# Kernel tuning notes

Hardware: AMD Instinct MI355X
Metric: run time of the kernel (lower is better)

## Reference

```python
import jax, jax.numpy as jnp
import numpy as np

N_NODES = 100000
N_EDGES = 3200000
NFEAT = 512
NCLASS = 40
DIMS = [NFEAT, 256, 128, 64, NCLASS]


def _glorot(key, fan_in, fan_out):
    lim = 1.0 / np.sqrt(fan_out)
    return jax.random.uniform(key, (fan_in, fan_out), jnp.float32, -lim, lim)


def setup_inputs() -> dict:
    key = jax.random.key(0)
    ks = jax.random.split(key, 16)
    inp = {
        'x': jax.random.normal(ks[0], (N_NODES, NFEAT), jnp.float32),
        'edge_src': jax.random.randint(ks[1], (N_EDGES,), 0, N_NODES, jnp.int32),
        'edge_dst': jax.random.randint(ks[2], (N_EDGES,), 0, N_NODES, jnp.int32),
        'edge_weight': jax.random.uniform(ks[3], (N_EDGES,), jnp.float32),
    }
    for i in range(4):
        inp[f'W{i+1}'] = _glorot(ks[4 + 2 * i], DIMS[i], DIMS[i + 1])
        lim = 1.0 / np.sqrt(DIMS[i + 1])
        inp[f'b{i+1}'] = jax.random.uniform(ks[5 + 2 * i], (DIMS[i + 1],), jnp.float32, -lim, lim)
    return inp


def _gc_layer(h, W, b, src, dst, ew):
    # support = h @ W ; out = spmm(adj, support) + b
    support = h @ W                                   # [N, d_out]
    msgs = support[src] * ew[:, None]                 # gather + scale per edge
    agg = jax.ops.segment_sum(msgs, dst, num_segments=N_NODES)
    return agg + b


def reference(x, edge_src, edge_dst, edge_weight, W1, b1, W2, b2, W3, b3, W4, b4):
    h = x
    for W, b in ((W1, b1), (W2, b2), (W3, b3), (W4, b4)):
        h = jax.nn.relu(_gc_layer(h, W, b, edge_src, edge_dst, edge_weight))
    return jax.nn.log_softmax(h, axis=1)
```

## Files before the change

kernel.cpp:

```cpp
#include <hip/hip_runtime.h>
#include <hip/hip_bf16.h>
#include <math.h>
#include <stdint.h>


#define WAVE 64
#define NBK 512
#define CHA 8192
typedef __attribute__((ext_vector_type(8))) short short8;
typedef __attribute__((ext_vector_type(8))) unsigned short ushort8;
typedef __attribute__((ext_vector_type(4))) unsigned int uintx4;
typedef __attribute__((ext_vector_type(4))) float floatx4;
typedef __attribute__((ext_vector_type(2))) float floatx2;

__device__ __forceinline__ void async_copy16(const void* g, void* l) {
    __builtin_amdgcn_global_load_lds(
        (const __attribute__((address_space(1))) void*)g,
        (__attribute__((address_space(3))) void*)l, 16, 0, 0);
}

__global__ __launch_bounds__(256) void prep_weights_kernel(
        const float* __restrict__ W1, const float* __restrict__ W2,
        const float* __restrict__ W3, const float* __restrict__ W4,
        const float* __restrict__ b4,
        __hip_bfloat16* __restrict__ Wt1, __hip_bfloat16* __restrict__ Wt2,
        __hip_bfloat16* __restrict__ Wt3, __hip_bfloat16* __restrict__ Wt4,
        float* __restrict__ b4p) {
    int idx = blockIdx.x * 256 + threadIdx.x;
    if (idx < 131072) {
        int n = idx >> 9, k = idx & 511;
        Wt1[idx] = __float2bfloat16(W1[(size_t)k * 256 + n]);
    } else if (idx < 131072 + 32768) {
        int l = idx - 131072;
        int n = l >> 8, k = l & 255;
        Wt2[l] = __float2bfloat16(W2[(size_t)k * 128 + n]);
    } else if (idx < 131072 + 32768 + 8192) {
        int l = idx - 131072 - 32768;
        int n = l >> 7, k = l & 127;
        Wt3[l] = __float2bfloat16(W3[(size_t)k * 64 + n]);
    } else if (idx < 131072 + 32768 + 8192 + 4096) {
        int l = idx - 131072 - 32768 - 8192;
        int n = l >> 6, k = l & 63;
        float v = (n < 40) ? W4[(size_t)k * 40 + n] : 0.f;
        Wt4[l] = __float2bfloat16(v);
    } else if (idx < 131072 + 32768 + 8192 + 4096 + 64) {
        int l = idx - 131072 - 32768 - 8192 - 4096;
        b4p[l] = (l < 40) ? b4[l] : 0.f;
    }
}


__global__ __launch_bounds__(256) void bucket_hist(const int* __restrict__ dst,
                                                   int nE, int* __restrict__ bhist) {
    __shared__ int h[NBK];
    const int t = threadIdx.x;
    const long e0 = (long)blockIdx.x * CHA;
    const int cnt = (int)((nE - e0 < CHA) ? (nE - e0) : CHA);
    for (int i = t; i < NBK; i += 256) h[i] = 0;
    __syncthreads();
    for (int i = t; i < cnt; i += 256)
        atomicAdd(&h[dst[e0 + i] >> 8], 1);
    __syncthreads();
    for (int i = t; i < NBK; i += 256)
        if (h[i]) atomicAdd(&bhist[i], h[i]);
}

__global__ __launch_bounds__(512) void bucket_scan(const int* __restrict__ bhist,
                                                   int* __restrict__ bbase,
                                                   int* __restrict__ gcur) {
    __shared__ int sm[NBK];
    const int t = threadIdx.x;
    int x = bhist[t];
    sm[t] = x;
    __syncthreads();
    for (int off = 1; off < NBK; off <<= 1) {
        int add = (t >= off) ? sm[t - off] : 0;
        __syncthreads();
        if (t >= off) sm[t] += add;
        __syncthreads();
    }
    int excl = sm[t] - x;
    bbase[t] = excl;
    gcur[t] = excl;
    if (t == NBK - 1) bbase[NBK] = sm[t];
}

__global__ __launch_bounds__(256) void scatter_phaseA(const int* __restrict__ src,
                                                      const int* __restrict__ dst,
                                                      const float* __restrict__ ew,
                                                      int nE,
                                                      int* __restrict__ gcur,
                                                      uint2* __restrict__ E2) {
    __shared__ int hist[NBK];
    __shared__ int cur[NBK];
    const int t = threadIdx.x;
    const long e0 = (long)blockIdx.x * CHA;
    const int cnt = (int)((nE - e0 < CHA) ? (nE - e0) : CHA);

    for (int i = t; i < NBK; i += 256) hist[i] = 0;
    __syncthreads();
    for (int i = t; i < cnt; i += 256)
        atomicAdd(&hist[dst[e0 + i] >> 8], 1);
    __syncthreads();
    for (int i = t; i < NBK; i += 256) {
        int h = hist[i];
        cur[i] = h ? atomicAdd(&gcur[i], h) : 0;
    }
    __syncthreads();
    for (int i = t; i < cnt; i += 256) {
        int d = dst[e0 + i];
        unsigned int w15 = (unsigned int)(ew[e0 + i] * 32767.f + 0.5f);
        if (w15 > 32767u) w15 = 32767u;
        int pos = atomicAdd(&cur[d >> 8], 1);
        E2[pos] = make_uint2(((unsigned int)src[e0 + i] << 15) | w15,
                             (unsigned int)d);
    }
}

__global__ __launch_bounds__(256) void scatter_phaseB2(const uint2* __restrict__ E2,
                                                       const int* __restrict__ bbase,
                                                       int n_nodes, int nE,
                                                       int* __restrict__ row_ptr,
                                                       unsigned int* __restrict__ edge_pk) {
    __shared__ int cnt[256];
    __shared__ int pfx[256];
    __shared__ int cur[256];
    const int b = blockIdx.x;
    const int t = threadIdx.x;
    const int s = bbase[b];
    const int e = bbase[b + 1];

    cnt[t] = 0;
    __syncthreads();
    for (int i = s + t; i < e; i += 256)
        atomicAdd(&cnt[E2[i].y & 255], 1);
    __syncthreads();
    pfx[t] = cnt[t];
    __syncthreads();
    for (int off = 1; off < 256; off <<= 1) {
        int add = (t >= off) ? pfx[t - off] : 0;
        __syncthreads();
        if (t >= off) pfx[t] += add;
        __syncthreads();
    }
    const int excl = pfx[t] - cnt[t];
    const int node = b * 256 + t;
    if (node < n_nodes) row_ptr[node] = s + excl;
    if (b == 0 && t == 0) row_ptr[n_nodes] = nE;
    cur[t] = s + excl;
    __syncthreads();
    for (int i = s + t; i < e; i += 256) {
        uint2 ed = E2[i];
        int p = atomicAdd(&cur[ed.y & 255], 1);
        edge_pk[p] = ed.x;
    }
}


template <int AFP32, int OUTM>
__global__ __launch_bounds__(256) void gemm128(const void* __restrict__ Av,
                                               const __hip_bfloat16* __restrict__ Wt,
                                               void* __restrict__ C,
                                               int M, int K, int Npitch) {
    __shared__ __align__(16) __hip_bfloat16 sA[128 * 64];
    __shared__ __align__(16) __hip_bfloat16 sB[128 * 64];
    const int t = threadIdx.x;
    const int lane = t & 63;
    const int w = t >> 6;
    const int wy = w >> 1, wx = w & 1;
    const int quad = lane >> 4;
    const int l16 = lane & 15;

    const int nwg = (int)(gridDim.x * gridDim.y);
    const int flat = (int)(blockIdx.y * gridDim.x + blockIdx.x);
    const int q = nwg >> 3, r = nwg & 7;
    const int xcd = flat & 7, pos = flat >> 3;
    const int logical = (xcd < r ? xcd * (q + 1) : r * (q + 1) + (xcd - r) * q) + pos;
    const int row0 = (logical / (int)gridDim.x) * 128;
    const int col0 = (logical % (int)gridDim.x) * 128;

    floatx4 acc[4][4];
#pragma unroll
    for (int mt = 0; mt < 4; mt++)
#pragma unroll
        for (int nt = 0; nt < 4; nt++) acc[mt][nt] = 0;

    const int arow = t >> 3;
    const int koff = (t & 7) * 8;

    float4 fa[4][2];
    auto loadA = [&](int k0) {
#pragma unroll
        for (int rr = 0; rr < 4; rr++) {
            int gm = row0 + rr * 32 + arow;
            int gmc = (gm < M) ? gm : 0;
            const float* ap = (const float*)Av + (size_t)gmc * K + k0 + koff;
            fa[rr][0] = *(const float4*)ap;
            fa[rr][1] = *(const float4*)(ap + 4);
        }
    };
    if (AFP32) loadA(0);

    for (int k0 = 0; k0 < K; k0 += 64) {
#pragma unroll
        for (int rr = 0; rr < 4; rr++) {
            int n = rr * 32 + arow;
            async_copy16(Wt + (size_t)(col0 + n) * K + k0 + koff,
                         (char*)sB + rr * 4096 + t * 16);
        }
        if (AFP32) {
#pragma unroll
            for (int rr = 0; rr < 4; rr++) {
                ushort8 pk;
#pragma unroll
                for (int i = 0; i < 4; i++) {
                    __hip_bfloat16 b0 = __float2bfloat16(((const float*)&fa[rr][0])[i]);
                    __hip_bfloat16 b1 = __float2bfloat16(((const float*)&fa[rr][1])[i]);
                    pk[i] = *(unsigned short*)&b0;
                    pk[4 + i] = *(unsigned short*)&b1;
                }
                *(ushort8*)((char*)sA + rr * 4096 + t * 16) = pk;
            }
        } else {
#pragma unroll
            for (int rr = 0; rr < 4; rr++) {
                int gm = row0 + rr * 32 + arow;
                int gmc = (gm < M) ? gm : 0;
                async_copy16((const __hip_bfloat16*)Av + (size_t)gmc * K + k0 + koff,
                             (char*)sA + rr * 4096 + t * 16);
            }
        }
        __syncthreads();

        if (AFP32 && k0 + 64 < K) loadA(k0 + 64);

        short8 af[4][2], bfr[4][2];
#pragma unroll
        for (int mt = 0; mt < 4; mt++)
#pragma unroll
            for (int kk = 0; kk < 2; kk++)
                af[mt][kk] = *(const short8*)((const char*)sA +
                             (wy * 64 + mt * 16 + l16) * 128 + kk * 64 + quad * 16);
#pragma unroll
        for (int nt = 0; nt < 4; nt++)
#pragma unroll
            for (int kk = 0; kk < 2; kk++)
                bfr[nt][kk] = *(const short8*)((const char*)sB +
                              (wx * 64 + nt * 16 + l16) * 128 + kk * 64 + quad * 16);
#pragma unroll
        for (int kk = 0; kk < 2; kk++)
#pragma unroll
            for (int mt = 0; mt < 4; mt++)
#pragma unroll
                for (int nt = 0; nt < 4; nt++)
                    acc[mt][nt] = __builtin_amdgcn_mfma_f32_16x16x32_bf16(
                        af[mt][kk], bfr[nt][kk], acc[mt][nt], 0, 0, 0);
        __syncthreads();
    }

#pragma unroll
    for (int mt = 0; mt < 4; mt++) {
#pragma unroll
        for (int nt = 0; nt < 4; nt++) {
            int gn = col0 + wx * 64 + nt * 16 + l16;
            int gmb = row0 + wy * 64 + mt * 16 + quad * 4;
#pragma unroll
            for (int rr = 0; rr < 4; rr++) {
                int gm = gmb + rr;
                if (gm < M) {
                    if (OUTM == 0) {
                        ((__hip_bfloat16*)C)[(size_t)gm * Npitch + gn] =
                            __float2bfloat16(acc[mt][nt][rr]);
                    } else {
                        float v = acc[mt][nt][rr];
                        int p = __builtin_amdgcn_cvt_pk_fp8_f32(v, v, 0, false);
                        ((unsigned char*)C)[(size_t)gm * Npitch + gn] =
                            (unsigned char)(p & 0xff);
                    }
                }
            }
        }
    }
}


template <int OUTM>
__global__ __launch_bounds__(256) void gemm_bf16(const __hip_bfloat16* __restrict__ A,
                                                 const __hip_bfloat16* __restrict__ Wt,
                                                 void* __restrict__ C,
                                                 int M, int K, int Npitch) {
    __shared__ __align__(16) __hip_bfloat16 sA[128 * 64];
    __shared__ __align__(16) __hip_bfloat16 sB[64 * 64];
    const int t = threadIdx.x;
    const int lane = t & 63;
    const int w = t >> 6;
    const int wy = w >> 1, wx = w & 1;
    const int quad = lane >> 4;
    const int l16 = lane & 15;
    const int row0 = blockIdx.y * 128;
    const int col0 = blockIdx.x * 64;

    floatx4 acc[4][2];
#pragma unroll
    for (int mt = 0; mt < 4; mt++)
#pragma unroll
        for (int nt = 0; nt < 2; nt++) acc[mt][nt] = 0;

    const int arow = t >> 3;
    const int koff = (t & 7) * 8;

    for (int k0 = 0; k0 < K; k0 += 64) {
#pragma unroll
        for (int r = 0; r < 4; r++) {
            int gm = row0 + r * 32 + arow;
            int gmc = (gm < M) ? gm : 0;
            async_copy16(A + (size_t)gmc * K + k0 + koff,
                         (char*)sA + r * 4096 + t * 16);
        }
#pragma unroll
        for (int r = 0; r < 2; r++) {
            int n = r * 32 + arow;
            async_copy16(Wt + (size_t)(col0 + n) * K + k0 + koff,
                         (char*)sB + r * 4096 + t * 16);
        }
        __syncthreads();

        short8 af[4][2], bfr[2][2];
#pragma unroll
        for (int mt = 0; mt < 4; mt++)
#pragma unroll
            for (int kk = 0; kk < 2; kk++)
                af[mt][kk] = *(const short8*)((const char*)sA +
                             (wy * 64 + mt * 16 + l16) * 128 + kk * 64 + quad * 16);
#pragma unroll
        for (int nt = 0; nt < 2; nt++)
#pragma unroll
            for (int kk = 0; kk < 2; kk++)
                bfr[nt][kk] = *(const short8*)((const char*)sB +
                              (wx * 32 + nt * 16 + l16) * 128 + kk * 64 + quad * 16);
#pragma unroll
        for (int kk = 0; kk < 2; kk++)
#pragma unroll
            for (int mt = 0; mt < 4; mt++)
#pragma unroll
                for (int nt = 0; nt < 2; nt++)
                    acc[mt][nt] = __builtin_amdgcn_mfma_f32_16x16x32_bf16(
                        af[mt][kk], bfr[nt][kk], acc[mt][nt], 0, 0, 0);
        __syncthreads();
    }

#pragma unroll
    for (int mt = 0; mt < 4; mt++) {
#pragma unroll
        for (int nt = 0; nt < 2; nt++) {
            int gn = col0 + wx * 32 + nt * 16 + l16;
            int gmb = row0 + wy * 64 + mt * 16 + quad * 4;
#pragma unroll
            for (int r = 0; r < 4; r++) {
                int gm = gmb + r;
                if (gm < M) {
                    if (OUTM == 0) {
                        ((__hip_bfloat16*)C)[(size_t)gm * Npitch + gn] =
                            __float2bfloat16(acc[mt][nt][r]);
                    } else {
                        float v = acc[mt][nt][r];
                        int p = __builtin_amdgcn_cvt_pk_fp8_f32(v, v, 0, false);
                        ((unsigned char*)C)[(size_t)gm * Npitch + gn] =
                            (unsigned char)(p & 0xff);
                    }
                }
            }
        }
    }
}


template <int D, int U, bool FINAL>
__global__ __launch_bounds__(256) void spmm_fp8(const int* __restrict__ row_ptr,
                                                const unsigned int* __restrict__ edge_pk,
                                                const unsigned char* __restrict__ sup8,
                                                const float* __restrict__ bias,
                                                void* __restrict__ out,
                                                int n_nodes) {
    constexpr int G = D / 16;
    constexpr int NG = 64 / G;
    constexpr int CH = NG * U;
    int node = blockIdx.x * (256 / WAVE) + (threadIdx.x >> 6);
    if (node >= n_nodes) return;
    node = __builtin_amdgcn_readfirstlane(node);
    const int lane = threadIdx.x & 63;
    const int g = lane / G;
    const int t = lane & (G - 1);
    int e = row_ptr[node];
    const int end = row_ptr[node + 1];
    const unsigned char* sup = sup8 + t * 16;

    float acc[16];
#pragma unroll
    for (int i = 0; i < 16; i++) acc[i] = 0.f;

    while (e < end) {
        const int base = e + g * U;
        unsigned int pk[U];
#pragma unroll
        for (int u = 0; u < U; u++) {
            int idx = base + u;
            if (idx > end - 1) idx = end - 1;
            pk[u] = edge_pk[idx];
        }
        uintx4 v[U];
#pragma unroll
        for (int u = 0; u < U; u++)
            v[u] = *(const uintx4*)(sup + (size_t)(pk[u] >> 15) * D);
#pragma unroll
        for (int u = 0; u < U; u++) {
            float wq = (float)(pk[u] & 0x7fffu) * (1.f / 32767.f);
            float wt = (base + u < end) ? wq : 0.f;
#pragma unroll
            for (int d = 0; d < 4; d++) {
                floatx2 lo = __builtin_amdgcn_cvt_pk_f32_fp8(v[u][d], false);
                floatx2 hi = __builtin_amdgcn_cvt_pk_f32_fp8(v[u][d], true);
                acc[d * 4 + 0] += lo[0] * wt;
                acc[d * 4 + 1] += lo[1] * wt;
                acc[d * 4 + 2] += hi[0] * wt;
                acc[d * 4 + 3] += hi[1] * wt;
            }
        }
        e += CH;
    }

#pragma unroll
    for (int off = G; off < 64; off <<= 1)
#pragma unroll
        for (int i = 0; i < 16; i++) acc[i] += __shfl_xor(acc[i], off);

    if (!FINAL) {
        if (lane < G) {
            ushort8 o0, o1;
#pragma unroll
            for (int i = 0; i < 8; i++) {
                float r0 = acc[i] + bias[t * 16 + i];
                float r1 = acc[8 + i] + bias[t * 16 + 8 + i];
                r0 = r0 > 0.f ? r0 : 0.f;
                r1 = r1 > 0.f ? r1 : 0.f;
                __hip_bfloat16 b0 = __float2bfloat16(r0);
                __hip_bfloat16 b1 = __float2bfloat16(r1);
                o0[i] = *(unsigned short*)&b0;
                o1[i] = *(unsigned short*)&b1;
            }
            union { ushort8 s; uintx4 u; } c0, c1; c0.s = o0; c1.s = o1;
            unsigned short* op = (unsigned short*)out + (size_t)node * D + t * 16;
            __builtin_nontemporal_store(c0.u, (uintx4*)op);
            __builtin_nontemporal_store(c1.u, (uintx4*)(op + 8));
        }
    } else {
        float r[16];
#pragma unroll
        for (int i = 0; i < 16; i++) {
            float x = acc[i] + bias[t * 16 + i];
            r[i] = x > 0.f ? x : 0.f;
        }
        float m = -INFINITY;
#pragma unroll
        for (int i = 0; i < 16; i++)
            if (t * 16 + i < 40) m = fmaxf(m, r[i]);
#pragma unroll
        for (int off = 1; off < G; off <<= 1) m = fmaxf(m, __shfl_xor(m, off));
        float s = 0.f;
#pragma unroll
        for (int i = 0; i < 16; i++)
            if (t * 16 + i < 40) s += __expf(r[i] - m);
#pragma unroll
        for (int off = 1; off < G; off <<= 1) s += __shfl_xor(s, off);
        const float lse = __logf(s);
        if (lane < G) {
            float* op = (float*)out + (size_t)node * 40;
#pragma unroll
            for (int i = 0; i < 16; i++) {
                int c = t * 16 + i;
                if (c < 40) op[c] = r[i] - m - lse;
            }
        }
    }
}


extern "C" void kernel_launch(void* const* d_in, const int* in_sizes, int n_in,
                              void* d_out, int out_size, void* d_ws, size_t ws_size,
                              hipStream_t stream) {
    const float* x    = (const float*)d_in[0];
    const int*   esrc = (const int*)d_in[1];
    const int*   edst = (const int*)d_in[2];
    const float* ew   = (const float*)d_in[3];
    const float* Wm[4] = {(const float*)d_in[4], (const float*)d_in[6],
                          (const float*)d_in[8], (const float*)d_in[10]};
    const float* bm[4] = {(const float*)d_in[5], (const float*)d_in[7],
                          (const float*)d_in[9], (const float*)d_in[11]};
    const int NFEAT = 512;
    const int n_nodes = in_sizes[0] / NFEAT;
    const int n_edges = in_sizes[1];
    float* out = (float*)d_out;

    char* wsp = (char*)d_ws;
    size_t off = 0;
    auto alloc = [&](size_t bytes) -> void* {
        void* p = wsp + off;
        off += (bytes + 255) & ~(size_t)255;
        return p;
    };
    __hip_bfloat16* Sb = (__hip_bfloat16*)alloc((size_t)n_nodes * 256 * sizeof(__hip_bfloat16));
    __hip_bfloat16* Hb = (__hip_bfloat16*)alloc((size_t)n_nodes * 256 * sizeof(__hip_bfloat16));
    __hip_bfloat16* Wt1 = (__hip_bfloat16*)alloc(256 * 512 * sizeof(__hip_bfloat16));
    __hip_bfloat16* Wt2 = (__hip_bfloat16*)alloc(128 * 256 * sizeof(__hip_bfloat16));
    __hip_bfloat16* Wt3 = (__hip_bfloat16*)alloc(64 * 128 * sizeof(__hip_bfloat16));
    __hip_bfloat16* Wt4 = (__hip_bfloat16*)alloc(64 * 64 * sizeof(__hip_bfloat16));
    float* b4p     = (float*)alloc(64 * sizeof(float));
    int*   row_ptr = (int*)alloc(((size_t)n_nodes + 1) * sizeof(int));
    int*   bhist   = (int*)alloc(NBK * sizeof(int));
    int*   bbase   = (int*)alloc((NBK + 1) * sizeof(int));
    int*   gcur    = (int*)alloc(NBK * sizeof(int));
    unsigned int* edge_pk = (unsigned int*)alloc((size_t)n_edges * sizeof(unsigned int));
    uint2* E2 = (uint2*)Hb;
    unsigned char* Sb8 = (unsigned char*)Sb;
    (void)ws_size;

    prep_weights_kernel<<<(131072 + 32768 + 8192 + 4096 + 64 + 255) / 256, 256, 0, stream>>>(
        Wm[0], Wm[1], Wm[2], Wm[3], bm[3], Wt1, Wt2, Wt3, Wt4, b4p);

    hipMemsetAsync(bhist, 0, NBK * sizeof(int), stream);
    int hblocks = (n_edges + CHA - 1) / CHA;
    bucket_hist<<<hblocks, 256, 0, stream>>>(edst, n_edges, bhist);
    bucket_scan<<<1, NBK, 0, stream>>>(bhist, bbase, gcur);
    scatter_phaseA<<<hblocks, 256, 0, stream>>>(esrc, edst, ew, n_edges, gcur, E2);
    scatter_phaseB2<<<NBK, 256, 0, stream>>>(E2, bbase, n_nodes, n_edges,
                                             row_ptr, edge_pk);

    int spmm_blocks = (n_nodes + 3) / 4;
    dim3 gg1(256 / 128, (n_nodes + 127) / 128);
    dim3 gg2(128 / 128, (n_nodes + 127) / 128);
    dim3 g3(64 / 64, (n_nodes + 127) / 128);

    gemm128<1, 1><<<gg1, 256, 0, stream>>>(x, Wt1, Sb8, n_nodes, 512, 256);
    spmm_fp8<256, 4, false><<<spmm_blocks, 256, 0, stream>>>(
        row_ptr, edge_pk, Sb8, bm[0], Hb, n_nodes);
    gemm128<0, 1><<<gg2, 256, 0, stream>>>(Hb, Wt2, Sb8, n_nodes, 256, 128);
    spmm_fp8<128, 2, false><<<spmm_blocks, 256, 0, stream>>>(
        row_ptr, edge_pk, Sb8, bm[1], Hb, n_nodes);
    gemm_bf16<1><<<g3, 256, 0, stream>>>(Hb, Wt3, Sb8, n_nodes, 128, 64);
    spmm_fp8<64, 1, false><<<spmm_blocks, 256, 0, stream>>>(
        row_ptr, edge_pk, Sb8, bm[2], Hb, n_nodes);
    gemm_bf16<1><<<g3, 256, 0, stream>>>(Hb, Wt4, Sb8, n_nodes, 64, 64);
    spmm_fp8<64, 1, true><<<spmm_blocks, 256, 0, stream>>>(
        row_ptr, edge_pk, Sb8, b4p, out, n_nodes);
}
```

Measured before the change: 817.7 us.

## Fuse edge scatter with first GEMM and histogram with weight prep

```diff
diff --git a/kernel.cpp b/kernel.cpp
--- a/kernel.cpp
+++ b/kernel.cpp
@@ -19,14 +19,29 @@
         (__attribute__((address_space(3))) void*)l, 16, 0, 0);
 }
 
-__global__ __launch_bounds__(256) void prep_weights_kernel(
+__global__ __launch_bounds__(256) void prep_hist_kernel(
+        const int* __restrict__ dst, int nE, int* __restrict__ bhist, int nH,
         const float* __restrict__ W1, const float* __restrict__ W2,
         const float* __restrict__ W3, const float* __restrict__ W4,
         const float* __restrict__ b4,
         __hip_bfloat16* __restrict__ Wt1, __hip_bfloat16* __restrict__ Wt2,
         __hip_bfloat16* __restrict__ Wt3, __hip_bfloat16* __restrict__ Wt4,
         float* __restrict__ b4p) {
-    int idx = blockIdx.x * 256 + threadIdx.x;
+    const int t = threadIdx.x;
+    if ((int)blockIdx.x < nH) {
+        __shared__ int h[NBK];
+        const long e0 = (long)blockIdx.x * CHA;
+        const int cnt = (int)((nE - e0 < CHA) ? (nE - e0) : CHA);
+        for (int i = t; i < NBK; i += 256) h[i] = 0;
+        __syncthreads();
+        for (int i = t; i < cnt; i += 256)
+            atomicAdd(&h[dst[e0 + i] >> 8], 1);
+        __syncthreads();
+        for (int i = t; i < NBK; i += 256)
+            if (h[i]) atomicAdd(&bhist[i], h[i]);
+        return;
+    }
+    int idx = ((int)blockIdx.x - nH) * 256 + t;
     if (idx < 131072) {
         int n = idx >> 9, k = idx & 511;
         Wt1[idx] = __float2bfloat16(W1[(size_t)k * 256 + n]);
@@ -49,22 +64,6 @@
     }
 }
 
-
-__global__ __launch_bounds__(256) void bucket_hist(const int* __restrict__ dst,
-                                                   int nE, int* __restrict__ bhist) {
-    __shared__ int h[NBK];
-    const int t = threadIdx.x;
-    const long e0 = (long)blockIdx.x * CHA;
-    const int cnt = (int)((nE - e0 < CHA) ? (nE - e0) : CHA);
-    for (int i = t; i < NBK; i += 256) h[i] = 0;
-    __syncthreads();
-    for (int i = t; i < cnt; i += 256)
-        atomicAdd(&h[dst[e0 + i] >> 8], 1);
-    __syncthreads();
-    for (int i = t; i < NBK; i += 256)
-        if (h[i]) atomicAdd(&bhist[i], h[i]);
-}
-
 __global__ __launch_bounds__(512) void bucket_scan(const int* __restrict__ bhist,
                                                    int* __restrict__ bbase,
                                                    int* __restrict__ gcur) {
@@ -85,39 +84,151 @@
     if (t == NBK - 1) bbase[NBK] = sm[t];
 }
 
-__global__ __launch_bounds__(256) void scatter_phaseA(const int* __restrict__ src,
-                                                      const int* __restrict__ dst,
-                                                      const float* __restrict__ ew,
-                                                      int nE,
-                                                      int* __restrict__ gcur,
-                                                      uint2* __restrict__ E2) {
-    __shared__ int hist[NBK];
-    __shared__ int cur[NBK];
+__global__ __launch_bounds__(256) void phaseA_gemm1(
+        const int* __restrict__ src, const int* __restrict__ dst,
+        const float* __restrict__ ew, int nE, int* __restrict__ gcur,
+        unsigned int* __restrict__ E2a, unsigned char* __restrict__ E2b,
+        int nA,
+        const float* __restrict__ X, const __hip_bfloat16* __restrict__ Wt,
+        unsigned char* __restrict__ C, int M, int K, int Npitch) {
+    __shared__ __align__(16) char smem[32768];
     const int t = threadIdx.x;
-    const long e0 = (long)blockIdx.x * CHA;
-    const int cnt = (int)((nE - e0 < CHA) ? (nE - e0) : CHA);
-
-    for (int i = t; i < NBK; i += 256) hist[i] = 0;
-    __syncthreads();
-    for (int i = t; i < cnt; i += 256)
-        atomicAdd(&hist[dst[e0 + i] >> 8], 1);
-    __syncthreads();
-    for (int i = t; i < NBK; i += 256) {
-        int h = hist[i];
-        cur[i] = h ? atomicAdd(&gcur[i], h) : 0;
-    }
-    __syncthreads();
-    for (int i = t; i < cnt; i += 256) {
-        int d = dst[e0 + i];
-        unsigned int w15 = (unsigned int)(ew[e0 + i] * 32767.f + 0.5f);
-        if (w15 > 32767u) w15 = 32767u;
-        int pos = atomicAdd(&cur[d >> 8], 1);
-        E2[pos] = make_uint2(((unsigned int)src[e0 + i] << 15) | w15,
-                             (unsigned int)d);
-    }
-}
-
-__global__ __launch_bounds__(256) void scatter_phaseB2(const uint2* __restrict__ E2,
+
+    if ((int)blockIdx.x < nA) {
+        int* hist = (int*)smem;
+        int* cur = hist + NBK;
+        const long e0 = (long)blockIdx.x * CHA;
+        const int cnt = (int)((nE - e0 < CHA) ? (nE - e0) : CHA);
+
+        for (int i = t; i < NBK; i += 256) hist[i] = 0;
+        __syncthreads();
+        for (int i = t; i < cnt; i += 256)
+            atomicAdd(&hist[dst[e0 + i] >> 8], 1);
+        __syncthreads();
+        for (int i = t; i < NBK; i += 256) {
+            int h = hist[i];
+            cur[i] = h ? atomicAdd(&gcur[i], h) : 0;
+        }
+        __syncthreads();
+        for (int i = t; i < cnt; i += 256) {
+            int d = dst[e0 + i];
+            unsigned int w15 = (unsigned int)(ew[e0 + i] * 32767.f + 0.5f);
+            if (w15 > 32767u) w15 = 32767u;
+            int pos = atomicAdd(&cur[d >> 8], 1);
+            E2a[pos] = ((unsigned int)src[e0 + i] << 15) | w15;
+            E2b[pos] = (unsigned char)(d & 255);
+        }
+        return;
+    }
+
+    __hip_bfloat16* sA = (__hip_bfloat16*)smem;
+    __hip_bfloat16* sB = (__hip_bfloat16*)(smem + 16384);
+    const int lane = t & 63;
+    const int w = t >> 6;
+    const int wy = w >> 1, wx = w & 1;
+    const int quad = lane >> 4;
+    const int l16 = lane & 15;
+
+    const int ntx = Npitch >> 7;
+    const int nty = (M + 127) >> 7;
+    const int nwg = ntx * nty;
+    const int flat = (int)blockIdx.x - nA;
+    const int q = nwg >> 3, r = nwg & 7;
+    const int xcd = flat & 7, pos = flat >> 3;
+    const int logical = (xcd < r ? xcd * (q + 1) : r * (q + 1) + (xcd - r) * q) + pos;
+    const int row0 = (logical / ntx) * 128;
+    const int col0 = (logical % ntx) * 128;
+
+    floatx4 acc[4][4];
+#pragma unroll
+    for (int mt = 0; mt < 4; mt++)
+#pragma unroll
+        for (int nt = 0; nt < 4; nt++) acc[mt][nt] = 0;
+
+    const int arow = t >> 3;
+    const int koff = (t & 7) * 8;
+
+    float4 fa[4][2];
+    auto loadA = [&](int k0) {
+#pragma unroll
+        for (int rr = 0; rr < 4; rr++) {
+            int gm = row0 + rr * 32 + arow;
+            int gmc = (gm < M) ? gm : 0;
+            const float* ap = X + (size_t)gmc * K + k0 + koff;
+            fa[rr][0] = *(const float4*)ap;
+            fa[rr][1] = *(const float4*)(ap + 4);
+        }
+    };
+    loadA(0);
+
+    for (int k0 = 0; k0 < K; k0 += 64) {
+#pragma unroll
+        for (int rr = 0; rr < 4; rr++) {
+            int n = rr * 32 + arow;
+            async_copy16(Wt + (size_t)(col0 + n) * K + k0 + koff,
+                         (char*)sB + rr * 4096 + t * 16);
+        }
+#pragma unroll
+        for (int rr = 0; rr < 4; rr++) {
+            ushort8 pk;
+#pragma unroll
+            for (int i = 0; i < 4; i++) {
+                __hip_bfloat16 b0 = __float2bfloat16(((const float*)&fa[rr][0])[i]);
+                __hip_bfloat16 b1 = __float2bfloat16(((const float*)&fa[rr][1])[i]);
+                pk[i] = *(unsigned short*)&b0;
+                pk[4 + i] = *(unsigned short*)&b1;
+            }
+            *(ushort8*)((char*)sA + rr * 4096 + t * 16) = pk;
+        }
+        __syncthreads();
+
+        if (k0 + 64 < K) loadA(k0 + 64);
+
+        short8 af[4][2], bfr[4][2];
+#pragma unroll
+        for (int mt = 0; mt < 4; mt++)
+#pragma unroll
+            for (int kk = 0; kk < 2; kk++)
+                af[mt][kk] = *(const short8*)((const char*)sA +
+                             (wy * 64 + mt * 16 + l16) * 128 + kk * 64 + quad * 16);
+#pragma unroll
+        for (int nt = 0; nt < 4; nt++)
+#pragma unroll
+            for (int kk = 0; kk < 2; kk++)
+                bfr[nt][kk] = *(const short8*)((const char*)sB +
+                              (wx * 64 + nt * 16 + l16) * 128 + kk * 64 + quad * 16);
+#pragma unroll
+        for (int kk = 0; kk < 2; kk++)
+#pragma unroll
+            for (int mt = 0; mt < 4; mt++)
+#pragma unroll
+                for (int nt = 0; nt < 4; nt++)
+                    acc[mt][nt] = __builtin_amdgcn_mfma_f32_16x16x32_bf16(
+                        af[mt][kk], bfr[nt][kk], acc[mt][nt], 0, 0, 0);
+        __syncthreads();
+    }
+
+#pragma unroll
+    for (int mt = 0; mt < 4; mt++) {
+#pragma unroll
+        for (int nt = 0; nt < 4; nt++) {
+            int gn = col0 + wx * 64 + nt * 16 + l16;
+            int gmb = row0 + wy * 64 + mt * 16 + quad * 4;
+#pragma unroll
+            for (int rr = 0; rr < 4; rr++) {
+                int gm = gmb + rr;
+                if (gm < M) {
+                    float v = acc[mt][nt][rr];
+                    int p = __builtin_amdgcn_cvt_pk_fp8_f32(v, v, 0, false);
+                    C[(size_t)gm * Npitch + gn] = (unsigned char)(p & 0xff);
+                }
+            }
+        }
+    }
+}
+
+__global__ __launch_bounds__(256) void scatter_phaseB2(const unsigned int* __restrict__ E2a,
+                                                       const unsigned char* __restrict__ E2b,
                                                        const int* __restrict__ bbase,
                                                        int n_nodes, int nE,
                                                        int* __restrict__ row_ptr,
@@ -133,7 +244,7 @@
     cnt[t] = 0;
     __syncthreads();
     for (int i = s + t; i < e; i += 256)
-        atomicAdd(&cnt[E2[i].y & 255], 1);
+        atomicAdd(&cnt[E2b[i]], 1);
     __syncthreads();
     pfx[t] = cnt[t];
     __syncthreads();
@@ -150,15 +261,14 @@
     cur[t] = s + excl;
     __syncthreads();
     for (int i = s + t; i < e; i += 256) {
-        uint2 ed = E2[i];
-        int p = atomicAdd(&cur[ed.y & 255], 1);
-        edge_pk[p] = ed.x;
-    }
-}
-
-
-template <int AFP32, int OUTM>
-__global__ __launch_bounds__(256) void gemm128(const void* __restrict__ Av,
+        int p = atomicAdd(&cur[E2b[i]], 1);
+        edge_pk[p] = E2a[i];
+    }
+}
+
+
+template <int OUTM>
+__global__ __launch_bounds__(256) void gemm128(const __hip_bfloat16* __restrict__ A,
                                                const __hip_bfloat16* __restrict__ Wt,
                                                void* __restrict__ C,
                                                int M, int K, int Npitch) {
@@ -188,19 +298,6 @@
     const int arow = t >> 3;
     const int koff = (t & 7) * 8;
 
-    float4 fa[4][2];
-    auto loadA = [&](int k0) {
-#pragma unroll
-        for (int rr = 0; rr < 4; rr++) {
-            int gm = row0 + rr * 32 + arow;
-            int gmc = (gm < M) ? gm : 0;
-            const float* ap = (const float*)Av + (size_t)gmc * K + k0 + koff;
-            fa[rr][0] = *(const float4*)ap;
-            fa[rr][1] = *(const float4*)(ap + 4);
-        }
-    };
-    if (AFP32) loadA(0);
-
     for (int k0 = 0; k0 < K; k0 += 64) {
 #pragma unroll
         for (int rr = 0; rr < 4; rr++) {
@@ -208,31 +305,14 @@
             async_copy16(Wt + (size_t)(col0 + n) * K + k0 + koff,
                          (char*)sB + rr * 4096 + t * 16);
         }
-        if (AFP32) {
-#pragma unroll
-            for (int rr = 0; rr < 4; rr++) {
-                ushort8 pk;
-#pragma unroll
-                for (int i = 0; i < 4; i++) {
-                    __hip_bfloat16 b0 = __float2bfloat16(((const float*)&fa[rr][0])[i]);
-                    __hip_bfloat16 b1 = __float2bfloat16(((const float*)&fa[rr][1])[i]);
-                    pk[i] = *(unsigned short*)&b0;
-                    pk[4 + i] = *(unsigned short*)&b1;
-                }
-                *(ushort8*)((char*)sA + rr * 4096 + t * 16) = pk;
-            }
-        } else {
-#pragma unroll
-            for (int rr = 0; rr < 4; rr++) {
-                int gm = row0 + rr * 32 + arow;
-                int gmc = (gm < M) ? gm : 0;
-                async_copy16((const __hip_bfloat16*)Av + (size_t)gmc * K + k0 + koff,
-                             (char*)sA + rr * 4096 + t * 16);
-            }
-        }
-        __syncthreads();
-
-        if (AFP32 && k0 + 64 < K) loadA(k0 + 64);
+#pragma unroll
+        for (int rr = 0; rr < 4; rr++) {
+            int gm = row0 + rr * 32 + arow;
+            int gmc = (gm < M) ? gm : 0;
+            async_copy16(A + (size_t)gmc * K + k0 + koff,
+                         (char*)sA + rr * 4096 + t * 16);
+        }
+        __syncthreads();
 
         short8 af[4][2], bfr[4][2];
 #pragma unroll
@@ -519,31 +599,35 @@
     int*   bhist   = (int*)alloc(NBK * sizeof(int));
     int*   bbase   = (int*)alloc((NBK + 1) * sizeof(int));
     int*   gcur    = (int*)alloc(NBK * sizeof(int));
-    unsigned int* edge_pk = (unsigned int*)alloc((size_t)n_edges * sizeof(unsigned int));
-    uint2* E2 = (uint2*)Hb;
+    unsigned int*  edge_pk = (unsigned int*)alloc((size_t)n_edges * sizeof(unsigned int));
+    unsigned char* E2b     = (unsigned char*)alloc((size_t)n_edges);
+    unsigned int* E2a = (unsigned int*)Hb;
     unsigned char* Sb8 = (unsigned char*)Sb;
     (void)ws_size;
 
-    prep_weights_kernel<<<(131072 + 32768 + 8192 + 4096 + 64 + 255) / 256, 256, 0, stream>>>(
+    const int nH = (n_edges + CHA - 1) / CHA;
+    const int nPrep = (131072 + 32768 + 8192 + 4096 + 64 + 255) / 256;
+
+    hipMemsetAsync(bhist, 0, NBK * sizeof(int), stream);
+    prep_hist_kernel<<<nH + nPrep, 256, 0, stream>>>(
+        edst, n_edges, bhist, nH,
         Wm[0], Wm[1], Wm[2], Wm[3], bm[3], Wt1, Wt2, Wt3, Wt4, b4p);
-
-    hipMemsetAsync(bhist, 0, NBK * sizeof(int), stream);
-    int hblocks = (n_edges + CHA - 1) / CHA;
-    bucket_hist<<<hblocks, 256, 0, stream>>>(edst, n_edges, bhist);
     bucket_scan<<<1, NBK, 0, stream>>>(bhist, bbase, gcur);
-    scatter_phaseA<<<hblocks, 256, 0, stream>>>(esrc, edst, ew, n_edges, gcur, E2);
-    scatter_phaseB2<<<NBK, 256, 0, stream>>>(E2, bbase, n_nodes, n_edges,
+
+    const int nty = (n_nodes + 127) / 128;
+    phaseA_gemm1<<<nH + 2 * nty, 256, 0, stream>>>(
+        esrc, edst, ew, n_edges, gcur, E2a, E2b, nH,
+        x, Wt1, Sb8, n_nodes, 512, 256);
+    scatter_phaseB2<<<NBK, 256, 0, stream>>>(E2a, E2b, bbase, n_nodes, n_edges,
                                              row_ptr, edge_pk);
 
     int spmm_blocks = (n_nodes + 3) / 4;
-    dim3 gg1(256 / 128, (n_nodes + 127) / 128);
-    dim3 gg2(128 / 128, (n_nodes + 127) / 128);
-    dim3 g3(64 / 64, (n_nodes + 127) / 128);
-
-    gemm128<1, 1><<<gg1, 256, 0, stream>>>(x, Wt1, Sb8, n_nodes, 512, 256);
+    dim3 gg2(1, nty);
+    dim3 g3(1, nty);
+
     spmm_fp8<256, 4, false><<<spmm_blocks, 256, 0, stream>>>(
         row_ptr, edge_pk, Sb8, bm[0], Hb, n_nodes);
-    gemm128<0, 1><<<gg2, 256, 0, stream>>>(Hb, Wt2, Sb8, n_nodes, 256, 128);
+    gemm128<1><<<gg2, 256, 0, stream>>>(Hb, Wt2, Sb8, n_nodes, 256, 128);
     spmm_fp8<128, 2, false><<<spmm_blocks, 256, 0, stream>>>(
         row_ptr, edge_pk, Sb8, bm[1], Hb, n_nodes);
     gemm_bf16<1><<<g3, 256, 0, stream>>>(Hb, Wt3, Sb8, n_nodes, 128, 64);
```

Measured after the change: 840.6 us. +2.8%, slower.
